# Kernel tuning notes

Measured on AMD Instinct MI355X. Metric: run time of the kernel, lower is better.

## Reference

```python
import jax, jax.numpy as jnp
import numpy as np
from jax import lax

WINDOW_SIZE = 11
SIGMA = 1.5
CHANNEL = 1
DATA_RANGE = 1.0
C1 = (0.01 * DATA_RANGE) ** 2
C2 = (0.03 * DATA_RANGE) ** 2


def _gaussian_window(size, sigma, channel):
    coords = jnp.arange(size, dtype=jnp.float32) - size // 2
    g = jnp.exp(-coords ** 2 / (2.0 * sigma ** 2))
    g = g / g.sum()
    w2d = g[:, None] * g[None, :]                    # (size, size)
    # depthwise weight layout OIHW: (channel, 1, size, size)
    return jnp.broadcast_to(w2d[None, None], (channel, 1, size, size))


def setup_inputs() -> dict:
    key = jax.random.key(0)
    k1, k2 = jax.random.split(key)
    B, C, H, W = 64, CHANNEL, 512, 512
    x = jax.random.uniform(k1, (B, C, H, W), dtype=jnp.float32)
    y = jax.random.uniform(k2, (B, C, H, W), dtype=jnp.float32)
    window = _gaussian_window(WINDOW_SIZE, SIGMA, CHANNEL)
    return {"x": x, "y": y, "window": window}


def _apply_window(t, window):
    pad = WINDOW_SIZE // 2
    return lax.conv_general_dilated(
        t, window,
        window_strides=(1, 1),
        padding=((pad, pad), (pad, pad)),
        dimension_numbers=("NCHW", "OIHW", "NCHW"),
        feature_group_count=CHANNEL,
    )


def reference(x, y, window):
    mu_x = _apply_window(x, window)
    mu_y = _apply_window(y, window)
    mu_x_sq = mu_x ** 2
    mu_y_sq = mu_y ** 2
    mu_xy = mu_x * mu_y
    sigma_x_sq = _apply_window(x * x, window) - mu_x_sq
    sigma_y_sq = _apply_window(y * y, window) - mu_y_sq
    sigma_xy = _apply_window(x * y, window) - mu_xy
    numerator = (2.0 * mu_xy + C1) * (2.0 * sigma_xy + C2)
    denominator = (mu_x_sq + mu_y_sq + C1) * (sigma_x_sq + sigma_y_sq + C2)
    ssim_map = numerator / denominator
    ssim_per_sample = ssim_map.mean(axis=(1, 2, 3))
    return ssim_per_sample.mean()  # reduction='mean'
```

## Files before the change

kernel.cpp:

```cpp
#include <hip/hip_runtime.h>


#define IMG 512
#define BH 32
#define CHUNK 4
#define NCHUNK (BH / CHUNK)
#define SROW 522
#define NTHREADS 512
#define GRIDX (IMG / BH)

typedef __attribute__((ext_vector_type(2))) float f32x2;

static __device__ __forceinline__ f32x2 pk_fma(f32x2 a, f32x2 b, f32x2 c) {
    f32x2 d;
    asm("v_pk_fma_f32 %0, %1, %2, %3" : "=v"(d) : "v"(a), "v"(b), "v"(c));
    return d;
}
static __device__ __forceinline__ f32x2 pk_mul(f32x2 a, f32x2 b) {
    f32x2 d;
    asm("v_pk_mul_f32 %0, %1, %2" : "=v"(d) : "v"(a), "v"(b));
    return d;
}

__global__ __launch_bounds__(NTHREADS, 4) void ssim_band(
    const float* __restrict__ x, const float* __restrict__ y,
    const float* __restrict__ win, float* __restrict__ partial)
{
    __shared__ __align__(16) f32x2 vab[CHUNK][SROW];
    __shared__ __align__(16) f32x2 vqq[CHUNK][SROW];
    __shared__ float sg[11];
    __shared__ float redbuf[NTHREADS / 64];

    const int tid = threadIdx.x;

    if (tid < 11) {
        float s = 0.f;
        #pragma unroll
        for (int j = 0; j < 11; ++j) s += win[tid * 11 + j];
        sg[tid] = s;
    }
    if (tid < 80) {
        int plane = tid / 40, rem = tid % 40, row = rem / 10, pc = rem % 10;
        int cc = (pc < 5) ? pc : (512 + pc);
        f32x2 z = (f32x2)(0.f);
        if (plane == 0) vab[row][cc] = z; else vqq[row][cc] = z;
    }

    const int y0 = blockIdx.x * BH;
    const size_t img_off = (size_t)blockIdx.y * (IMG * IMG);
    const float* __restrict__ xb = x + img_off + tid;
    const float* __restrict__ yb = y + img_off + tid;

    f32x2 pab[14];
    #pragma unroll
    for (int j = 0; j < 10; ++j) {
        int gy = y0 - 5 + j;
        float a = 0.f, b = 0.f;
        if (gy >= 0) { a = xb[gy * IMG]; b = yb[gy * IMG]; }
        pab[j][0] = a + b;
        pab[j][1] = a - b;
    }

    __syncthreads();
    f32x2 g2[11];
    #pragma unroll
    for (int k = 0; k < 11; ++k) { float gv = sg[k]; g2[k][0] = gv; g2[k][1] = gv; }

    const float C1 = 1.0e-4f;
    const float C2 = 9.0e-4f;
    float acc = 0.f;

    const int rr = tid & 3;
    const int c0 = (tid >> 2) * 4;

    for (int k = 0; k < NCHUNK; ++k) {
        const int r0 = y0 + k * CHUNK;

        #pragma unroll
        for (int j = 0; j < 4; ++j) {
            int gy = r0 + 5 + j;
            float a = 0.f, b = 0.f;
            if (gy < IMG) { a = xb[gy * IMG]; b = yb[gy * IMG]; }
            pab[10 + j][0] = a + b;
            pab[10 + j][1] = a - b;
        }

        f32x2 sq[14];
        #pragma unroll
        for (int j = 0; j < 14; ++j) sq[j] = pk_mul(pab[j], pab[j]);

        #pragma unroll
        for (int i = 0; i < CHUNK; ++i) {
            f32x2 a = (f32x2)(0.f), q = (f32x2)(0.f);
            #pragma unroll
            for (int t = 0; t < 11; ++t) {
                a = pk_fma(g2[t], pab[i + t], a);
                q = pk_fma(g2[t], sq[i + t], q);
            }
            vab[i][tid + 5] = a;
            vqq[i][tid + 5] = q;
        }

        __syncthreads();

        {
            f32x2 mu[4], qq[4];
            {
                f32x2 t[14];
                const float4* p = (const float4*)&vab[rr][c0];
                #pragma unroll
                for (int q8 = 0; q8 < 7; ++q8) {
                    float4 f = p[q8];
                    t[2*q8][0] = f.x;  t[2*q8][1] = f.y;
                    t[2*q8+1][0] = f.z;  t[2*q8+1][1] = f.w;
                }
                #pragma unroll
                for (int i = 0; i < 4; ++i) {
                    f32x2 a = (f32x2)(0.f);
                    #pragma unroll
                    for (int t1 = 0; t1 < 11; ++t1) a = pk_fma(g2[t1], t[i + t1], a);
                    mu[i] = a;
                }
            }
            {
                f32x2 t[14];
                const float4* p = (const float4*)&vqq[rr][c0];
                #pragma unroll
                for (int q8 = 0; q8 < 7; ++q8) {
                    float4 f = p[q8];
                    t[2*q8][0] = f.x;  t[2*q8][1] = f.y;
                    t[2*q8+1][0] = f.z;  t[2*q8+1][1] = f.w;
                }
                #pragma unroll
                for (int i = 0; i < 4; ++i) {
                    f32x2 a = (f32x2)(0.f);
                    #pragma unroll
                    for (int t1 = 0; t1 < 11; ++t1) a = pk_fma(g2[t1], t[i + t1], a);
                    qq[i] = a;
                }
            }

            #pragma unroll
            for (int i = 0; i < 4; ++i) {
                f32x2 m2 = pk_mul(mu[i], mu[i]);
                float P = m2[0] + m2[1];
                float Q = m2[0] - m2[1];
                float R = qq[i][0] + qq[i][1];
                float S = qq[i][0] - qq[i][1];
                float num1 = fmaf(0.5f, Q, C1);
                float num2 = fmaf(0.5f, S - Q, C2);
                float den1 = fmaf(0.5f, P, C1);
                float den2 = fmaf(0.5f, R - P, C2);
                acc += (num1 * num2) * __builtin_amdgcn_rcpf(den1 * den2);
            }
        }

        __syncthreads();

        #pragma unroll
        for (int j = 0; j < 10; ++j) pab[j] = pab[j + 4];
    }

    #pragma unroll
    for (int off = 32; off > 0; off >>= 1) acc += __shfl_down(acc, off, 64);
    int wid = tid >> 6, lane = tid & 63;
    if (lane == 0) redbuf[wid] = acc;
    __syncthreads();
    if (tid == 0) {
        float ssum = 0.f;
        #pragma unroll
        for (int w = 0; w < NTHREADS / 64; ++w) ssum += redbuf[w];
        partial[blockIdx.y * gridDim.x + blockIdx.x] = ssum;
    }
}

__global__ __launch_bounds__(512) void ssim_finalize(
    const float* __restrict__ partial, float* __restrict__ out)
{
    __shared__ double red[8];
    double acc = (double)partial[threadIdx.x] + (double)partial[threadIdx.x + 512];
    #pragma unroll
    for (int off = 32; off > 0; off >>= 1) acc += __shfl_down(acc, off, 64);
    int wid = threadIdx.x >> 6, lane = threadIdx.x & 63;
    if (lane == 0) red[wid] = acc;
    __syncthreads();
    if (threadIdx.x == 0) {
        double ssum = 0.0;
        #pragma unroll
        for (int w = 0; w < 8; ++w) ssum += red[w];
        out[0] = (float)(ssum / (64.0 * 512.0 * 512.0));
    }
}

extern "C" void kernel_launch(void* const* d_in, const int* in_sizes, int n_in,
                              void* d_out, int out_size, void* d_ws, size_t ws_size,
                              hipStream_t stream) {
    (void)in_sizes; (void)n_in; (void)out_size; (void)ws_size;
    const float* x   = (const float*)d_in[0];
    const float* y   = (const float*)d_in[1];
    const float* win = (const float*)d_in[2];
    float* out = (float*)d_out;
    float* partial = (float*)d_ws;

    dim3 grid(GRIDX, 64);
    ssim_band<<<grid, NTHREADS, 0, stream>>>(x, y, win, partial);
    ssim_finalize<<<1, 512, 0, stream>>>(partial, out);
}
```

Before: 170.3 us.

## Double-buffer shared vertical-pass planes to drop one barrier per chunk

Adds a second pair of shared-memory buffers so each chunk's vertical convolution writes into one buffer while the horizontal pass reads the other. This removes one of the two __syncthreads per chunk and lets the vertical compute of chunk k+1 overlap with the horizontal compute of chunk k across waves. The cost is doubled LDS use (about 67KB per block), which may cut the occupancy set by the launch bounds of 4 blocks, and a prologue that computes the first chunk ahead of the loop.

```diff
diff --git a/kernel.cpp b/kernel.cpp
--- a/kernel.cpp
+++ b/kernel.cpp
@@ -26,8 +26,10 @@
     const float* __restrict__ x, const float* __restrict__ y,
     const float* __restrict__ win, float* __restrict__ partial)
 {
-    __shared__ __align__(16) f32x2 vab[CHUNK][SROW];
-    __shared__ __align__(16) f32x2 vqq[CHUNK][SROW];
+    __shared__ __align__(16) f32x2 vab0[CHUNK][SROW];
+    __shared__ __align__(16) f32x2 vqq0[CHUNK][SROW];
+    __shared__ __align__(16) f32x2 vab1[CHUNK][SROW];
+    __shared__ __align__(16) f32x2 vqq1[CHUNK][SROW];
     __shared__ float sg[11];
     __shared__ float redbuf[NTHREADS / 64];
 
@@ -39,11 +41,13 @@
         for (int j = 0; j < 11; ++j) s += win[tid * 11 + j];
         sg[tid] = s;
     }
-    if (tid < 80) {
-        int plane = tid / 40, rem = tid % 40, row = rem / 10, pc = rem % 10;
+    if (tid < 160) {
+        int buf = tid / 80, rem = tid % 80;
+        int plane = rem / 40, rem2 = rem % 40, row = rem2 / 10, pc = rem2 % 10;
         int cc = (pc < 5) ? pc : (512 + pc);
         f32x2 z = (f32x2)(0.f);
-        if (plane == 0) vab[row][cc] = z; else vqq[row][cc] = z;
+        if (buf == 0) { if (plane == 0) vab0[row][cc] = z; else vqq0[row][cc] = z; }
+        else          { if (plane == 0) vab1[row][cc] = z; else vqq1[row][cc] = z; }
     }
 
     const int y0 = blockIdx.x * BH;
@@ -53,7 +57,7 @@
 
     f32x2 pab[14];
     #pragma unroll
-    for (int j = 0; j < 10; ++j) {
+    for (int j = 0; j < 14; ++j) {
         int gy = y0 - 5 + j;
         float a = 0.f, b = 0.f;
         if (gy >= 0) { a = xb[gy * IMG]; b = yb[gy * IMG]; }
@@ -66,6 +70,24 @@
     #pragma unroll
     for (int k = 0; k < 11; ++k) { float gv = sg[k]; g2[k][0] = gv; g2[k][1] = gv; }
 
+    {
+        f32x2 sq[14];
+        #pragma unroll
+        for (int j = 0; j < 14; ++j) sq[j] = pk_mul(pab[j], pab[j]);
+        #pragma unroll
+        for (int i = 0; i < CHUNK; ++i) {
+            f32x2 a = (f32x2)(0.f), q = (f32x2)(0.f);
+            #pragma unroll
+            for (int t = 0; t < 11; ++t) {
+                a = pk_fma(g2[t], pab[i + t], a);
+                q = pk_fma(g2[t], sq[i + t], q);
+            }
+            vab0[i][tid + 5] = a;
+            vqq0[i][tid + 5] = q;
+        }
+    }
+    __syncthreads();
+
     const float C1 = 1.0e-4f;
     const float C2 = 9.0e-4f;
     float acc = 0.f;
@@ -73,41 +95,42 @@
     const int rr = tid & 3;
     const int c0 = (tid >> 2) * 4;
 
-    for (int k = 0; k < NCHUNK; ++k) {
-        const int r0 = y0 + k * CHUNK;
-
-        #pragma unroll
-        for (int j = 0; j < 4; ++j) {
-            int gy = r0 + 5 + j;
-            float a = 0.f, b = 0.f;
-            if (gy < IMG) { a = xb[gy * IMG]; b = yb[gy * IMG]; }
-            pab[10 + j][0] = a + b;
-            pab[10 + j][1] = a - b;
+    auto span = [&](int k,
+                    f32x2 (&rab)[CHUNK][SROW], f32x2 (&rqq)[CHUNK][SROW],
+                    f32x2 (&wab)[CHUNK][SROW], f32x2 (&wqq)[CHUNK][SROW]) {
+        if (k < NCHUNK - 1) {
+            #pragma unroll
+            for (int j = 0; j < 10; ++j) pab[j] = pab[j + 4];
+            int rbase = y0 + 4 * k + 9;
+            #pragma unroll
+            for (int j = 0; j < 4; ++j) {
+                int gy = rbase + j;
+                float a = 0.f, b = 0.f;
+                if (gy < IMG) { a = xb[gy * IMG]; b = yb[gy * IMG]; }
+                pab[10 + j][0] = a + b;
+                pab[10 + j][1] = a - b;
+            }
+            f32x2 sq[14];
+            #pragma unroll
+            for (int j = 0; j < 14; ++j) sq[j] = pk_mul(pab[j], pab[j]);
+            #pragma unroll
+            for (int i = 0; i < CHUNK; ++i) {
+                f32x2 a = (f32x2)(0.f), q = (f32x2)(0.f);
+                #pragma unroll
+                for (int t = 0; t < 11; ++t) {
+                    a = pk_fma(g2[t], pab[i + t], a);
+                    q = pk_fma(g2[t], sq[i + t], q);
+                }
+                wab[i][tid + 5] = a;
+                wqq[i][tid + 5] = q;
+            }
         }
-
-        f32x2 sq[14];
-        #pragma unroll
-        for (int j = 0; j < 14; ++j) sq[j] = pk_mul(pab[j], pab[j]);
-
-        #pragma unroll
-        for (int i = 0; i < CHUNK; ++i) {
-            f32x2 a = (f32x2)(0.f), q = (f32x2)(0.f);
-            #pragma unroll
-            for (int t = 0; t < 11; ++t) {
-                a = pk_fma(g2[t], pab[i + t], a);
-                q = pk_fma(g2[t], sq[i + t], q);
-            }
-            vab[i][tid + 5] = a;
-            vqq[i][tid + 5] = q;
-        }
-
-        __syncthreads();
 
         {
             f32x2 mu[4], qq[4];
             {
                 f32x2 t[14];
-                const float4* p = (const float4*)&vab[rr][c0];
+                const float4* p = (const float4*)&rab[rr][c0];
                 #pragma unroll
                 for (int q8 = 0; q8 < 7; ++q8) {
                     float4 f = p[q8];
@@ -124,7 +147,7 @@
             }
             {
                 f32x2 t[14];
-                const float4* p = (const float4*)&vqq[rr][c0];
+                const float4* p = (const float4*)&rqq[rr][c0];
                 #pragma unroll
                 for (int q8 = 0; q8 < 7; ++q8) {
                     float4 f = p[q8];
@@ -155,10 +178,13 @@
             }
         }
 
-        __syncthreads();
-
-        #pragma unroll
-        for (int j = 0; j < 10; ++j) pab[j] = pab[j + 4];
+        if (k < NCHUNK - 1) __syncthreads();
+    };
+
+    #pragma unroll 1
+    for (int kk = 0; kk < NCHUNK; kk += 2) {
+        span(kk,     vab0, vqq0, vab1, vqq1);
+        span(kk + 1, vab1, vqq1, vab0, vqq0);
     }
 
     #pragma unroll
```

Result: faster. 166.1 us (-2.5%).
